# Kernel tuning notes

Measured on AMD Instinct MI355X. Metric: run time of the kernel, lower is better.

The kernel has to match this reference:

```python
import jax, jax.numpy as jnp
import numpy as np

D_K = 64

def setup_inputs() -> dict:
    key = jax.random.key(0)
    k1, k2, k3, k4 = jax.random.split(key, 4)
    hidden_states = jax.random.normal(k1, (2, 16, 128, 16, 16), dtype=jnp.float32)
    # nn.Linear(hidden, d, bias=False); stored as [in, out] for x @ W
    w_q = jax.random.normal(k2, (128, 64), dtype=jnp.float32) * 0.05
    w_k = jax.random.normal(k3, (128, 64), dtype=jnp.float32) * 0.05
    w_v = jax.random.normal(k4, (128, 64), dtype=jnp.float32) * 0.05
    return {"hidden_states": hidden_states, "w_q": w_q, "w_k": w_k, "w_v": w_v}

def reference(hidden_states, w_q, w_k, w_v):
    # (B, T, C, H, W) -> (B, T, H, W, C) -> (N, C)
    x = jnp.transpose(hidden_states, (0, 1, 3, 4, 2))
    x = x.reshape(-1, x.shape[-1])                      # [N, C], N = B*T*H*W
    q = x @ w_q                                          # [N, d_k]
    k = x @ w_k                                          # [N, d_k]
    v = x @ w_v                                          # [N, d_v]
    scores = (q @ k.T) / jnp.sqrt(jnp.asarray(D_K, x.dtype))  # [N, N]
    attn = jax.nn.softmax(scores, axis=1)                # softmax over dim=1
    out = attn @ v                                       # [N, d_v]
    return out
```

## Files before the change

kernel.cpp:

```cpp
#include <hip/hip_runtime.h>
#include <hip/hip_bf16.h>

typedef float f32x4 __attribute__((ext_vector_type(4)));
typedef short bf16x8 __attribute__((ext_vector_type(8)));

#define MFMA32 __builtin_amdgcn_mfma_f32_16x16x32_bf16

__device__ __forceinline__ unsigned short f2bf(float f) {
  union { float f; unsigned u; } v; v.f = f;
  unsigned u = v.u;
  u += 0x7FFFu + ((u >> 16) & 1u);
  return (unsigned short)(u >> 16);
}

__device__ __forceinline__ bf16x8 pack8_bf16(float a, float b, float c, float d,
                                             float e, float f, float g, float h) {
  union { bf16x8 v; __hip_bfloat162 p[4]; } u;
  u.p[0] = __float22bfloat162_rn(make_float2(a, b));
  u.p[1] = __float22bfloat162_rn(make_float2(c, d));
  u.p[2] = __float22bfloat162_rn(make_float2(e, f));
  u.p[3] = __float22bfloat162_rn(make_float2(g, h));
  return u.v;
}

__device__ __forceinline__ void stage16(const unsigned short* gbase,
                                        unsigned short* lbase, int lane) {
#if __has_builtin(__builtin_amdgcn_global_load_lds)
  __builtin_amdgcn_global_load_lds(
      (const __attribute__((address_space(1))) void*)(gbase + lane * 8),
      (__attribute__((address_space(3))) void*)lbase, 16, 0, 0);
#else
  *(bf16x8*)(lbase + lane * 8) = *(const bf16x8*)(gbase + lane * 8);
#endif
}

__global__ __launch_bounds__(256) void qkv_kernel(
    const float* __restrict__ hs,
    const float* __restrict__ wq, const float* __restrict__ wk,
    const float* __restrict__ wv,
    unsigned short* __restrict__ qb, unsigned short* __restrict__ kpack,
    unsigned short* __restrict__ vpack)
{
  __shared__ __align__(16) float Wl[128 * 64];
  __shared__ float xs[32 * 129];
  const int t = threadIdx.x;
  const int mat = blockIdx.y;
  const float* __restrict__ W = (mat == 0) ? wq : (mat == 1) ? wk : wv;
  #pragma unroll
  for (int i = 0; i < 8; ++i) {
    *(f32x4*)(Wl + i * 1024 + t * 4) = *(const f32x4*)(W + i * 1024 + t * 4);
  }
  const int n0 = blockIdx.x * 32;
  const int bt = n0 >> 8;
  const int sp0 = n0 & 255;
  {
    const float* __restrict__ src = hs + (size_t)bt * 32768 + sp0;
    const int s = t & 31, cb = t >> 5;
    #pragma unroll
    for (int i = 0; i < 16; ++i) {
      const int c = i * 8 + cb;
      xs[s * 129 + c] = src[c * 256 + s];
    }
  }
  __syncthreads();
  const int s = t & 31, g = t >> 5;
  float acc[8];
  #pragma unroll
  for (int j = 0; j < 8; ++j) acc[j] = 0.f;
  #pragma unroll 4
  for (int c = 0; c < 128; ++c) {
    const float xv = xs[s * 129 + c];
    const f32x4 w0 = *(const f32x4*)(Wl + c * 64 + g * 8);
    const f32x4 w1 = *(const f32x4*)(Wl + c * 64 + g * 8 + 4);
    acc[0] += xv * w0[0]; acc[1] += xv * w0[1];
    acc[2] += xv * w0[2]; acc[3] += xv * w0[3];
    acc[4] += xv * w1[0]; acc[5] += xv * w1[1];
    acc[6] += xv * w1[2]; acc[7] += xv * w1[3];
  }
  const int n = n0 + s;
  const float SCALE = 1.4426950408889634f / 8.0f;
  if (mat == 0) {
    #pragma unroll
    for (int j = 0; j < 8; ++j) qb[n * 64 + g * 8 + j] = f2bf(acc[j] * SCALE);
  } else if (mat == 1) {
    const int kvb32 = n >> 5, kvl = n & 31;
    const int ti = (kvl >> 2) & 1;
    const int lowk = ((kvl >> 3) << 2) | (kvl & 3);
    const int h = g >> 2, quadk = g & 3;
    unsigned short* dst =
        kpack + (((size_t)(kvb32 * 2 + ti) * 2 + h) * 64 + quadk * 16 + lowk) * 8;
    #pragma unroll
    for (int j = 0; j < 8; ++j) dst[j] = f2bf(acc[j]);
  } else {
    const int kvb32 = n >> 5, kvl = n & 31;
    const int quadv = kvl >> 3, jj = kvl & 7;
    #pragma unroll
    for (int jw = 0; jw < 8; ++jw) {
      const int d = g * 8 + jw, dt = d >> 4, lowd = d & 15;
      vpack[(((size_t)kvb32 * 4 + dt) * 64 + quadv * 16 + lowd) * 8 + jj] =
          f2bf(acc[jw]);
    }
  }
}

__global__ __launch_bounds__(256, 4) void flash_kernel(
    const unsigned short* __restrict__ qb,
    const unsigned short* __restrict__ kpack,
    const unsigned short* __restrict__ vpack,
    float* __restrict__ opart, float* __restrict__ lpart, int kvlen, int G)
{
  __shared__ __align__(16) unsigned short Kl[2][2][2048];
  __shared__ __align__(16) unsigned short Vl[2][2][2048];
  const int t = threadIdx.x;
  const int w = t >> 6, lane = t & 63;
  const int quad = lane >> 4, low = lane & 15;
  const int bid = blockIdx.x;
  const int g = bid % G;
  const int qblk = bid / G;
  const int q0 = qblk * 128 + w * 32;
  const int kvb32_0 = (g * kvlen) >> 5;
  const int nch = kvlen >> 6;

  bf16x8 bq[2][2];
  #pragma unroll
  for (int qt = 0; qt < 2; ++qt)
    #pragma unroll
    for (int h = 0; h < 2; ++h)
      bq[qt][h] = *(const bf16x8*)(qb + (q0 + qt * 16 + low) * 64 + h * 32 + quad * 8);

  f32x4 O[2][4];
  f32x4 O4[2];
  #pragma unroll
  for (int qt = 0; qt < 2; ++qt) {
    #pragma unroll
    for (int dt = 0; dt < 4; ++dt) O[qt][dt] = (f32x4){0.f, 0.f, 0.f, 0.f};
    O4[qt] = (f32x4){0.f, 0.f, 0.f, 0.f};
  }
  const bf16x8 ones = {16256, 16256, 16256, 16256, 16256, 16256, 16256, 16256};

  #define STAGE_CHUNK(b, c)                                                   \
    {                                                                         \
      const int kb32 = w >> 1, hf = w & 1;                                    \
      const size_t kb = (size_t)(kvb32_0 + (c) * 2 + kb32) * 2048;            \
      _Pragma("unroll")                                                       \
      for (int r = 0; r < 2; ++r) {                                           \
        const int fo = (hf * 2 + r) * 512;                                    \
        stage16(kpack + kb + fo, &Kl[b][kb32][fo], lane);                     \
        stage16(vpack + kb + fo, &Vl[b][kb32][fo], lane);                     \
      }                                                                       \
    }

  STAGE_CHUNK(0, 0)
  __syncthreads();

  for (int c = 0; c < nch; ++c) {
    const int b = c & 1;
    if (c + 1 < nch) STAGE_CHUNK(b ^ 1, c + 1)
    #pragma unroll
    for (int j = 0; j < 2; ++j) {
      bf16x8 kf[4], vf[4];
      #pragma unroll
      for (int f = 0; f < 4; ++f)
        kf[f] = *(const bf16x8*)&Kl[b][j][f * 512 + lane * 8];
      #pragma unroll
      for (int f = 0; f < 4; ++f)
        vf[f] = *(const bf16x8*)&Vl[b][j][f * 512 + lane * 8];
      #pragma unroll
      for (int qt = 0; qt < 2; ++qt) {
        f32x4 SA = {0.f, 0.f, 0.f, 0.f}, SB = {0.f, 0.f, 0.f, 0.f};
        SA = MFMA32(kf[0], bq[qt][0], SA, 0, 0, 0);
        SA = MFMA32(kf[1], bq[qt][1], SA, 0, 0, 0);
        SB = MFMA32(kf[2], bq[qt][0], SB, 0, 0, 0);
        SB = MFMA32(kf[3], bq[qt][1], SB, 0, 0, 0);
        const float pa0 = __builtin_amdgcn_exp2f(SA[0]);
        const float pa1 = __builtin_amdgcn_exp2f(SA[1]);
        const float pa2 = __builtin_amdgcn_exp2f(SA[2]);
        const float pa3 = __builtin_amdgcn_exp2f(SA[3]);
        const float pb0 = __builtin_amdgcn_exp2f(SB[0]);
        const float pb1 = __builtin_amdgcn_exp2f(SB[1]);
        const float pb2 = __builtin_amdgcn_exp2f(SB[2]);
        const float pb3 = __builtin_amdgcn_exp2f(SB[3]);
        const bf16x8 pf = pack8_bf16(pa0, pa1, pa2, pa3, pb0, pb1, pb2, pb3);
        #pragma unroll
        for (int dt = 0; dt < 4; ++dt)
          O[qt][dt] = MFMA32(vf[dt], pf, O[qt][dt], 0, 0, 0);
        O4[qt] = MFMA32(ones, pf, O4[qt], 0, 0, 0);
      }
    }
    __syncthreads();
  }
  #undef STAGE_CHUNK

  #pragma unroll
  for (int qt = 0; qt < 2; ++qt) {
    const size_t qrow = (size_t)g * 8192 + q0 + qt * 16;
    #pragma unroll
    for (int dt = 0; dt < 4; ++dt)
      *(f32x4*)(opart + (qrow + low) * 64 + dt * 16 + quad * 4) = O[qt][dt];
    if (quad == 0) lpart[qrow + low] = O4[qt][0];
  }
}

__global__ __launch_bounds__(256) void reduce_kernel(
    const float* __restrict__ opart, const float* __restrict__ lpart,
    float* __restrict__ out, int G)
{
  const int idx = blockIdx.x * 256 + threadIdx.x;
  const int q = idx >> 4;
  const int d4 = (idx & 15) * 4;
  f32x4 n0 = {0.f, 0.f, 0.f, 0.f}, n1 = n0, n2 = n0, n3 = n0;
  float d0 = 0.f, d1 = 0.f, d2 = 0.f, d3 = 0.f;
  int g = 0;
  for (; g + 4 <= G; g += 4) {
    const size_t r0 = (size_t)(g + 0) * 8192 + q;
    const size_t r1 = (size_t)(g + 1) * 8192 + q;
    const size_t r2 = (size_t)(g + 2) * 8192 + q;
    const size_t r3 = (size_t)(g + 3) * 8192 + q;
    d0 += lpart[r0]; d1 += lpart[r1]; d2 += lpart[r2]; d3 += lpart[r3];
    n0 += *(const f32x4*)(opart + r0 * 64 + d4);
    n1 += *(const f32x4*)(opart + r1 * 64 + d4);
    n2 += *(const f32x4*)(opart + r2 * 64 + d4);
    n3 += *(const f32x4*)(opart + r3 * 64 + d4);
  }
  for (; g < G; ++g) {
    const size_t r0 = (size_t)g * 8192 + q;
    d0 += lpart[r0];
    n0 += *(const f32x4*)(opart + r0 * 64 + d4);
  }
  const float den = (d0 + d1) + (d2 + d3);
  const f32x4 num = (n0 + n1) + (n2 + n3);
  const float r = 1.0f / den;
  *(f32x4*)(out + (size_t)q * 64 + d4) = num * r;
}

extern "C" void kernel_launch(void* const* d_in, const int* in_sizes, int n_in,
                              void* d_out, int out_size, void* d_ws, size_t ws_size,
                              hipStream_t stream) {
  const float* hs = (const float*)d_in[0];
  const float* wq = (const float*)d_in[1];
  const float* wk = (const float*)d_in[2];
  const float* wv = (const float*)d_in[3];
  float* out = (float*)d_out;
  char* ws = (char*)d_ws;

  unsigned short* qb    = (unsigned short*)ws;
  unsigned short* kpack = (unsigned short*)(ws + (1 << 20));
  unsigned short* vpack = (unsigned short*)(ws + (2 << 20));

  int G = 16;
  {
    const size_t per_g = (size_t)8192 * 64 * 4 + (size_t)8192 * 4;
    while (G > 1 && ws_size < (size_t)(3 << 20) + (size_t)G * per_g) G >>= 1;
  }
  float* opart = (float*)(ws + (3 << 20));
  float* lpart = (float*)(ws + (3 << 20) + (size_t)G * 8192 * 64 * 4);

  qkv_kernel<<<dim3(256, 3, 1), 256, 0, stream>>>(hs, wq, wk, wv, qb, kpack, vpack);
  flash_kernel<<<64 * G, 256, 0, stream>>>(qb, kpack, vpack, opart, lpart,
                                           8192 / G, G);
  reduce_kernel<<<512, 256, 0, stream>>>(opart, lpart, out, G);
}
```

Before: 98.25 us.

## Use 512-thread blocks with triple-buffered async KV staging and single barrier

Doubles the flash block to 8 waves covering 256 query rows, so each staged K/V chunk is shared by twice as many queries, and halves the grid. LDS staging becomes a three-deep ring where each wave loads one 512-element slice, synchronized with explicit vmcnt waits and one s_barrier per chunk instead of two __syncthreads. This is meant to cut global/LDS staging traffic per query and the barrier stalls. In exchange the kernel relies on stage16 being the only outstanding vector-memory op per iteration for the vmcnt(2) count to be correct, and it uses more LDS per block.

```diff
diff --git a/kernel.cpp b/kernel.cpp
--- a/kernel.cpp
+++ b/kernel.cpp
@@ -103,21 +103,21 @@
   }
 }
 
-__global__ __launch_bounds__(256, 4) void flash_kernel(
+__global__ __launch_bounds__(512, 4) void flash_kernel(
     const unsigned short* __restrict__ qb,
     const unsigned short* __restrict__ kpack,
     const unsigned short* __restrict__ vpack,
     float* __restrict__ opart, float* __restrict__ lpart, int kvlen, int G)
 {
-  __shared__ __align__(16) unsigned short Kl[2][2][2048];
-  __shared__ __align__(16) unsigned short Vl[2][2][2048];
+  __shared__ __align__(16) unsigned short Kl[3][4096];
+  __shared__ __align__(16) unsigned short Vl[3][4096];
   const int t = threadIdx.x;
   const int w = t >> 6, lane = t & 63;
   const int quad = lane >> 4, low = lane & 15;
   const int bid = blockIdx.x;
   const int g = bid % G;
   const int qblk = bid / G;
-  const int q0 = qblk * 128 + w * 32;
+  const int q0 = qblk * 256 + w * 32;
   const int kvb32_0 = (g * kvlen) >> 5;
   const int nch = kvlen >> 6;
 
@@ -140,31 +140,31 @@
 
   #define STAGE_CHUNK(b, c)                                                   \
     {                                                                         \
-      const int kb32 = w >> 1, hf = w & 1;                                    \
-      const size_t kb = (size_t)(kvb32_0 + (c) * 2 + kb32) * 2048;            \
-      _Pragma("unroll")                                                       \
-      for (int r = 0; r < 2; ++r) {                                           \
-        const int fo = (hf * 2 + r) * 512;                                    \
-        stage16(kpack + kb + fo, &Kl[b][kb32][fo], lane);                     \
-        stage16(vpack + kb + fo, &Vl[b][kb32][fo], lane);                     \
-      }                                                                       \
+      const size_t kb = (size_t)(kvb32_0 + (c) * 2) * 2048 + w * 512;         \
+      stage16(kpack + kb, &Kl[b][w * 512], lane);                             \
+      stage16(vpack + kb, &Vl[b][w * 512], lane);                             \
     }
 
   STAGE_CHUNK(0, 0)
-  __syncthreads();
+  STAGE_CHUNK(1, 1)
 
   for (int c = 0; c < nch; ++c) {
-    const int b = c & 1;
-    if (c + 1 < nch) STAGE_CHUNK(b ^ 1, c + 1)
+    if (c + 1 < nch) asm volatile("s_waitcnt vmcnt(2)" ::: "memory");
+    else             asm volatile("s_waitcnt vmcnt(0)" ::: "memory");
+    __builtin_amdgcn_s_barrier();
+    if (c + 2 < nch) STAGE_CHUNK((c + 2) % 3, c + 2)
+
+    const unsigned short* __restrict__ Kb = Kl[c % 3];
+    const unsigned short* __restrict__ Vb = Vl[c % 3];
     #pragma unroll
     for (int j = 0; j < 2; ++j) {
       bf16x8 kf[4], vf[4];
       #pragma unroll
       for (int f = 0; f < 4; ++f)
-        kf[f] = *(const bf16x8*)&Kl[b][j][f * 512 + lane * 8];
+        kf[f] = *(const bf16x8*)&Kb[j * 2048 + f * 512 + lane * 8];
       #pragma unroll
       for (int f = 0; f < 4; ++f)
-        vf[f] = *(const bf16x8*)&Vl[b][j][f * 512 + lane * 8];
+        vf[f] = *(const bf16x8*)&Vb[j * 2048 + f * 512 + lane * 8];
       #pragma unroll
       for (int qt = 0; qt < 2; ++qt) {
         f32x4 SA = {0.f, 0.f, 0.f, 0.f}, SB = {0.f, 0.f, 0.f, 0.f};
@@ -187,7 +187,6 @@
         O4[qt] = MFMA32(ones, pf, O4[qt], 0, 0, 0);
       }
     }
-    __syncthreads();
   }
   #undef STAGE_CHUNK
 
@@ -256,7 +255,7 @@
   float* lpart = (float*)(ws + (3 << 20) + (size_t)G * 8192 * 64 * 4);
 
   qkv_kernel<<<dim3(256, 3, 1), 256, 0, stream>>>(hs, wq, wk, wv, qb, kpack, vpack);
-  flash_kernel<<<64 * G, 256, 0, stream>>>(qb, kpack, vpack, opart, lpart,
+  flash_kernel<<<32 * G, 512, 0, stream>>>(qb, kpack, vpack, opart, lpart,
                                            8192 / G, G);
   reduce_kernel<<<512, 256, 0, stream>>>(opart, lpart, out, G);
 }
```

Measured after the change: 100.3 us. +2.1%, slower.
